# Kernel optimization log

Measured on AMD Instinct MI355X. Metric: run time of the kernel, lower is better.

The kernel has to match this reference:

```python
import jax, jax.numpy as jnp
import numpy as np

B = 16384
INPUT_DIM = 256
NUM_SLOTS = 32
SLOT_DIM = 64
NUM_KNOWN = 9
HIDDEN = 128
ITERS = 3
LN_EPS = 1e-5


def _lin(k, fan_in, w_shape, b_shape):
    # torch nn.Linear default init: U(-1/sqrt(fan_in), 1/sqrt(fan_in))
    bound = 1.0 / np.sqrt(fan_in)
    k1, k2 = jax.random.split(k)
    W = jax.random.uniform(k1, w_shape, jnp.float32, -bound, bound)
    b = jax.random.uniform(k2, b_shape, jnp.float32, -bound, bound)
    return W, b


def setup_inputs() -> dict:
    key = jax.random.key(0)
    ks = jax.random.split(key, 20)
    inp = {}
    inp['world_state'] = jax.random.normal(ks[0], (B, INPUT_DIM), jnp.float32)
    inp['eps'] = jax.random.normal(ks[1], (B, NUM_SLOTS, SLOT_DIM), jnp.float32)
    inp['slots_mu'] = jax.random.normal(ks[2], (1, NUM_SLOTS, SLOT_DIM), jnp.float32)
    inp['slots_sigma'] = jnp.ones((1, NUM_SLOTS, SLOT_DIM), jnp.float32) * 0.1
    inp['Wi'], inp['bi'] = _lin(ks[3], INPUT_DIM, (INPUT_DIM, SLOT_DIM), (SLOT_DIM,))
    inp['Wk'], inp['bk'] = _lin(ks[4], SLOT_DIM, (SLOT_DIM, SLOT_DIM), (SLOT_DIM,))
    inp['Wq'], inp['bq'] = _lin(ks[5], SLOT_DIM, (SLOT_DIM, SLOT_DIM), (SLOT_DIM,))
    inp['Wv'], inp['bv'] = _lin(ks[6], SLOT_DIM, (SLOT_DIM, SLOT_DIM), (SLOT_DIM,))
    inp['W_ih'], inp['b_ih'] = _lin(ks[7], SLOT_DIM, (SLOT_DIM, 3 * SLOT_DIM), (3 * SLOT_DIM,))
    inp['W_hh'], inp['b_hh'] = _lin(ks[8], SLOT_DIM, (SLOT_DIM, 3 * SLOT_DIM), (3 * SLOT_DIM,))
    inp['W1'], inp['b1'] = _lin(ks[9], SLOT_DIM, (SLOT_DIM, HIDDEN), (HIDDEN,))
    inp['W2'], inp['b2'] = _lin(ks[10], HIDDEN, (HIDDEN, SLOT_DIM), (SLOT_DIM,))
    inp['g_in'] = jnp.ones((SLOT_DIM,), jnp.float32)
    inp['b_in'] = jnp.zeros((SLOT_DIM,), jnp.float32)
    inp['g_sl'] = jnp.ones((SLOT_DIM,), jnp.float32)
    inp['b_sl'] = jnp.zeros((SLOT_DIM,), jnp.float32)
    inp['g_mlp'] = jnp.ones((SLOT_DIM,), jnp.float32)
    inp['b_mlp'] = jnp.zeros((SLOT_DIM,), jnp.float32)
    inp['Wh1'], inp['bh1'] = _lin(ks[11], SLOT_DIM, (NUM_KNOWN, SLOT_DIM, SLOT_DIM // 2), (NUM_KNOWN, SLOT_DIM // 2))
    inp['Wh2'], inp['bh2'] = _lin(ks[12], SLOT_DIM // 2, (NUM_KNOWN, SLOT_DIM // 2), (NUM_KNOWN,))
    return inp


def _ln(x, g, b):
    mu = jnp.mean(x, axis=-1, keepdims=True)
    var = jnp.mean(jnp.square(x - mu), axis=-1, keepdims=True)
    return (x - mu) / jnp.sqrt(var + LN_EPS) * g + b


def reference(world_state, eps, slots_mu, slots_sigma, Wi, bi, Wk, bk, Wq, bq, Wv, bv,
              W_ih, b_ih, W_hh, b_hh, W1, b1, W2, b2,
              g_in, b_in, g_sl, b_sl, g_mlp, b_mlp, Wh1, bh1, Wh2, bh2):
    scale = SLOT_DIM ** (-0.5)
    x = world_state[:, None, :] @ Wi + bi            # [B,1,D]
    x = _ln(x, g_in, b_in)
    k = x @ Wk + bk                                   # [B,1,D] (loop-invariant)
    v = x @ Wv + bv                                   # [B,1,D]
    slots = slots_mu + slots_sigma * eps              # [B,S,D]
    for _ in range(ITERS):
        prev = slots
        sn = _ln(slots, g_sl, b_sl)
        q = sn @ Wq + bq                              # [B,S,D]
        attn = jnp.einsum('bnd,bsd->bns', k, q) * scale  # [B,1,S]
        attn = jax.nn.softmax(attn, axis=-1) + 1e-8
        attn = attn / jnp.sum(attn, axis=1, keepdims=True)  # dual normalization
        upd = jnp.einsum('bns,bnd->bsd', attn, v)     # [B,S,D]
        # GRUCell
        gi = upd @ W_ih + b_ih                        # [B,S,3D]
        gh = prev @ W_hh + b_hh
        r = jax.nn.sigmoid(gi[..., :SLOT_DIM] + gh[..., :SLOT_DIM])
        z = jax.nn.sigmoid(gi[..., SLOT_DIM:2 * SLOT_DIM] + gh[..., SLOT_DIM:2 * SLOT_DIM])
        n = jnp.tanh(gi[..., 2 * SLOT_DIM:] + r * gh[..., 2 * SLOT_DIM:])
        slots = (1.0 - z) * n + z * prev
        # residual MLP
        h = _ln(slots, g_mlp, b_mlp)
        slots = slots + jax.nn.gelu(h @ W1 + b1, approximate=False) @ W2 + b2
    # known property heads (vectorized over 9 heads)
    s9 = slots[:, :NUM_KNOWN, :]                      # [B,9,D]
    hh = jax.nn.gelu(jnp.einsum('bkd,kdh->bkh', s9, Wh1) + bh1, approximate=False)
    pv = jax.nn.sigmoid(jnp.einsum('bkh,kh->bk', hh, Wh2) + bh2)  # [B,9]
    free_act = jnp.sqrt(jnp.sum(jnp.square(slots[:, NUM_KNOWN:, :]), axis=-1)).mean(axis=0)  # [num_free]
    return (pv, slots, free_act)
```

## Files before the change

### kernel.cpp

```cpp
#include <hip/hip_runtime.h>


typedef __attribute__((ext_vector_type(4))) float f32x4;
typedef __attribute__((ext_vector_type(8))) short s16x8;

#define MFMA16 __builtin_amdgcn_mfma_f32_16x16x32_bf16

#define NB       16384
#define GIB_OFF  (32 + 120*256)
#define PV_N     147456
#define SLOT_N   33554432

__device__ __forceinline__ unsigned short f2bf(float f){
  unsigned int u = __builtin_bit_cast(unsigned int, f);
  u += 0x7fffu + ((u >> 16) & 1u);
  return (unsigned short)(u >> 16);
}
__device__ __forceinline__ float bf2f(unsigned short s){
  unsigned int u = ((unsigned int)s) << 16;
  return __builtin_bit_cast(float, u);
}
__device__ __forceinline__ float sigm(float x){
  return __builtin_amdgcn_rcpf(1.f + __expf(-x));
}
__device__ __forceinline__ float tanh_(float x){
  return 1.f - 2.f*__builtin_amdgcn_rcpf(1.f + __expf(2.f*x));
}
__device__ __forceinline__ float geluf(float x){
  return x * sigm(1.5957691216f*x*(1.f + 0.044715f*x*x));
}

__global__ void prep1_pack(const float* __restrict__ Wi, const float* __restrict__ Wv,
                           const float* __restrict__ Wih, const float* __restrict__ Whh,
                           const float* __restrict__ W1, const float* __restrict__ W2,
                           float* __restrict__ wsf){
  int t = blockIdx.x*256 + threadIdx.x;
  if (blockIdx.x == 0 && threadIdx.x < 32) wsf[threadIdx.x] = 0.f;
  if (t >= 120*64) return;
  int frag = t >> 6, lane = t & 63;
  int q = lane >> 4, idx = lane & 15;
  const float* W; int ncols, ct, kf;
  if      (frag < 24){ W=Whh; ncols=192; ct=frag>>1;      kf=frag&1; }
  else if (frag < 40){ int f=frag-24; W=W1;  ncols=128; ct=f>>1; kf=f&1; }
  else if (frag < 56){ int f=frag-40; W=W2;  ncols=64;  ct=f>>2; kf=f&3; }
  else if (frag < 88){ int f=frag-56; W=Wi;  ncols=64;  ct=f>>3; kf=f&7; }
  else if (frag < 96){ int f=frag-88; W=Wv;  ncols=64;  ct=f>>1; kf=f&1; }
  else               { int f=frag-96; W=Wih; ncols=192; ct=f>>1; kf=f&1; }
  int k0 = kf*32 + q*8;
  int n  = ct*16 + idx;
  unsigned short* dst = (unsigned short*)(wsf + 32) + frag*512 + lane*8;
  #pragma unroll
  for (int j = 0; j < 8; ++j) dst[j] = f2bf(W[(size_t)(k0+j)*ncols + n]);
}

__global__ __launch_bounds__(256) void prep2_gi(
    const float* __restrict__ wstate, const float* __restrict__ bi,
    const float* __restrict__ bv, const float* __restrict__ bih,
    const float* __restrict__ g_in, const float* __restrict__ b_in,
    float* __restrict__ wsf){
  __shared__ __align__(16) unsigned short sxn[4][1152];
  const f32x4 zf = {0.f,0.f,0.f,0.f};
  int tid = threadIdx.x;
  int w = __builtin_amdgcn_readfirstlane(tid >> 6);
  int lane = tid & 63, q = lane >> 4, idx = lane & 15;
  int br0 = blockIdx.x*64 + w*16;
  const unsigned short* fb = (const unsigned short*)(wsf + 32);
  float* gib = wsf + GIB_OFF;

  s16x8 af[8];
  #pragma unroll
  for (int kf = 0; kf < 8; ++kf){
    const float* src = wstate + (size_t)(br0+idx)*256 + kf*32 + q*8;
    f32x4 p0 = *(const f32x4*)(src);
    f32x4 p1 = *(const f32x4*)(src+4);
    s16x8 a;
    a[0]=(short)f2bf(p0[0]); a[1]=(short)f2bf(p0[1]); a[2]=(short)f2bf(p0[2]); a[3]=(short)f2bf(p0[3]);
    a[4]=(short)f2bf(p1[0]); a[5]=(short)f2bf(p1[1]); a[6]=(short)f2bf(p1[2]); a[7]=(short)f2bf(p1[3]);
    af[kf] = a;
  }
  float xv[4][4];
  #pragma unroll
  for (int ct = 0; ct < 4; ++ct){
    f32x4 acc = zf;
    #pragma unroll
    for (int kf = 0; kf < 8; ++kf)
      acc = MFMA16(af[kf], *(const s16x8*)(fb + (56 + ct*8 + kf)*512 + lane*8), acc, 0,0,0);
    float bb = bi[ct*16+idx];
    #pragma unroll
    for (int e = 0; e < 4; ++e) xv[ct][e] = acc[e] + bb;
  }
  #pragma unroll
  for (int e = 0; e < 4; ++e){
    float s1 = xv[0][e]+xv[1][e]+xv[2][e]+xv[3][e];
    float s2 = xv[0][e]*xv[0][e]+xv[1][e]*xv[1][e]+xv[2][e]*xv[2][e]+xv[3][e]*xv[3][e];
    #pragma unroll
    for (int m = 1; m < 16; m <<= 1){ s1 += __shfl_xor(s1,m); s2 += __shfl_xor(s2,m); }
    float mean = s1*(1.f/64.f);
    float var  = s2*(1.f/64.f) - mean*mean;
    float rs   = __builtin_amdgcn_rsqf(var + 1e-5f);
    #pragma unroll
    for (int ct = 0; ct < 4; ++ct){
      int c = ct*16+idx;
      sxn[w][(q*4+e)*72 + c] = f2bf((xv[ct][e]-mean)*rs*g_in[c] + b_in[c]);
    }
  }
  s16x8 xa0 = *(const s16x8*)(&sxn[w][idx*72 + q*8]);
  s16x8 xa1 = *(const s16x8*)(&sxn[w][idx*72 + 32 + q*8]);
  #pragma unroll
  for (int ct = 0; ct < 4; ++ct){
    f32x4 acc = MFMA16(xa0, *(const s16x8*)(fb + (88 + ct*2 + 0)*512 + lane*8), zf, 0,0,0);
    acc       = MFMA16(xa1, *(const s16x8*)(fb + (88 + ct*2 + 1)*512 + lane*8), acc, 0,0,0);
    float bb = bv[ct*16+idx];
    #pragma unroll
    for (int e = 0; e < 4; ++e) sxn[w][(q*4+e)*72 + ct*16+idx] = f2bf(acc[e] + bb);
  }
  s16x8 va0 = *(const s16x8*)(&sxn[w][idx*72 + q*8]);
  s16x8 va1 = *(const s16x8*)(&sxn[w][idx*72 + 32 + q*8]);
  #pragma unroll
  for (int ct = 0; ct < 12; ++ct){
    f32x4 acc = MFMA16(va0, *(const s16x8*)(fb + (96 + ct*2 + 0)*512 + lane*8), zf, 0,0,0);
    acc       = MFMA16(va1, *(const s16x8*)(fb + (96 + ct*2 + 1)*512 + lane*8), acc, 0,0,0);
    float bb = bih[ct*16+idx];
    #pragma unroll
    for (int e = 0; e < 4; ++e)
      gib[(size_t)(br0 + q*4 + e)*192 + ct*16 + idx] = acc[e] + bb;
  }
}

__global__ __launch_bounds__(256, 2) void bank_main(
    const float* __restrict__ eps, const float* __restrict__ smu, const float* __restrict__ ssig,
    const float* __restrict__ bhh, const float* __restrict__ b1v, const float* __restrict__ b2v,
    const float* __restrict__ g_mlp, const float* __restrict__ b_mlp,
    const float* __restrict__ Wh1, const float* __restrict__ bh1,
    const float* __restrict__ Wh2, const float* __restrict__ bh2,
    float* __restrict__ wsf, float* __restrict__ out){
  __shared__ __align__(16) unsigned short swgt[20480];
  __shared__ __align__(16) unsigned short sbuf[4][2176];
  __shared__ float sgi[2][192];
  __shared__ float sbias[512];
  __shared__ float sfree[2][24];
  const f32x4 zf = {0.f,0.f,0.f,0.f};
  int tid = threadIdx.x;
  int w = __builtin_amdgcn_readfirstlane(tid >> 6);
  int lane = tid & 63, q = lane >> 4, idx = lane & 15;
  int pair = w >> 1, half = w & 1;
  int b = blockIdx.x*2 + pair;
  const unsigned short* fb = (const unsigned short*)(wsf + 32);
  const float* gib = wsf + GIB_OFF;

  {
    const uint4* src = (const uint4*)fb;
    uint4* dst = (uint4*)swgt;
    #pragma unroll
    for (int i = 0; i < 10; ++i) dst[tid + 256*i] = src[tid + 256*i];
  }
  for (int i = tid; i < 512; i += 256){
    float vv;
    if      (i < 192) vv = bhh[i];
    else if (i < 320) vv = b1v[i-192];
    else if (i < 384) vv = b2v[i-320];
    else if (i < 448) vv = g_mlp[i-384];
    else              vv = b_mlp[i-448];
    sbias[i] = vv;
  }
  if (half == 0){
    #pragma unroll
    for (int jj = 0; jj < 3; ++jj) sgi[pair][jj*64+lane] = gib[(size_t)b*192 + jj*64 + lane];
  }
  unsigned short* S = &sbuf[w][0];
  int s0 = half*16;
  #pragma unroll
  for (int rr = 0; rr < 16; ++rr){
    int s = s0 + rr;
    float ev = eps[((size_t)b*32 + s)*64 + lane];
    S[rr*136 + lane] = f2bf(smu[s*64+lane] + ssig[s*64+lane]*ev);
  }
  __syncthreads();

  size_t obase = (size_t)PV_N + ((size_t)b*32 + s0)*64;
  #pragma unroll 1
  for (int it = 0; it < 3; ++it){
    s16x8 a0 = *(const s16x8*)(&S[idx*136 + q*8]);
    s16x8 a1 = *(const s16x8*)(&S[idx*136 + 32 + q*8]);
    f32x4 gacc[12];
    #pragma unroll
    for (int ct = 0; ct < 12; ++ct){
      f32x4 acc = MFMA16(a0, *(const s16x8*)(&swgt[(ct*2+0)*512 + lane*8]), zf, 0,0,0);
      gacc[ct]  = MFMA16(a1, *(const s16x8*)(&swgt[(ct*2+1)*512 + lane*8]), acc, 0,0,0);
    }
    float nsv[4][4];
    #pragma unroll
    for (int ct = 0; ct < 4; ++ct){
      int c = ct*16+idx;
      float bhr = sbias[c], bhz = sbias[64+c], bhn = sbias[128+c];
      float gir = sgi[pair][c], giz = sgi[pair][64+c], gin = sgi[pair][128+c];
      #pragma unroll
      for (int e = 0; e < 4; ++e){
        float r = sigm(gir + gacc[ct][e] + bhr);
        float z = sigm(giz + gacc[4+ct][e] + bhz);
        float n = tanh_(gin + r*(gacc[8+ct][e] + bhn));
        float prev = bf2f(S[(q*4+e)*136 + c]);
        nsv[ct][e] = (1.f - z)*n + z*prev;
      }
    }
    #pragma unroll
    for (int e = 0; e < 4; ++e){
      float s1 = nsv[0][e]+nsv[1][e]+nsv[2][e]+nsv[3][e];
      float s2 = nsv[0][e]*nsv[0][e]+nsv[1][e]*nsv[1][e]+nsv[2][e]*nsv[2][e]+nsv[3][e]*nsv[3][e];
      #pragma unroll
      for (int m = 1; m < 16; m <<= 1){ s1 += __shfl_xor(s1,m); s2 += __shfl_xor(s2,m); }
      float mean = s1*(1.f/64.f);
      float var  = s2*(1.f/64.f) - mean*mean;
      float rs   = __builtin_amdgcn_rsqf(var + 1e-5f);
      #pragma unroll
      for (int ct = 0; ct < 4; ++ct){
        int c = ct*16+idx;
        S[(q*4+e)*136 + c] = f2bf((nsv[ct][e]-mean)*rs*sbias[384+c] + sbias[448+c]);
      }
    }
    s16x8 h0 = *(const s16x8*)(&S[idx*136 + q*8]);
    s16x8 h1 = *(const s16x8*)(&S[idx*136 + 32 + q*8]);
    f32x4 macc[8];
    #pragma unroll
    for (int ct = 0; ct < 8; ++ct){
      f32x4 acc = MFMA16(h0, *(const s16x8*)(&swgt[(24+ct*2+0)*512 + lane*8]), zf, 0,0,0);
      macc[ct]  = MFMA16(h1, *(const s16x8*)(&swgt[(24+ct*2+1)*512 + lane*8]), acc, 0,0,0);
    }
    #pragma unroll
    for (int ct = 0; ct < 8; ++ct){
      int c = ct*16+idx;
      float bb = sbias[192+c];
      #pragma unroll
      for (int e = 0; e < 4; ++e)
        S[(q*4+e)*136 + c] = f2bf(geluf(macc[ct][e] + bb));
    }
    s16x8 t0 = *(const s16x8*)(&S[idx*136 +       q*8]);
    s16x8 t1 = *(const s16x8*)(&S[idx*136 + 32  + q*8]);
    s16x8 t2 = *(const s16x8*)(&S[idx*136 + 64  + q*8]);
    s16x8 t3 = *(const s16x8*)(&S[idx*136 + 96  + q*8]);
    #pragma unroll
    for (int ct = 0; ct < 4; ++ct){
      f32x4 acc = MFMA16(t0, *(const s16x8*)(fb + (40+ct*4+0)*512 + lane*8), zf, 0,0,0);
      acc       = MFMA16(t1, *(const s16x8*)(fb + (40+ct*4+1)*512 + lane*8), acc, 0,0,0);
      acc       = MFMA16(t2, *(const s16x8*)(fb + (40+ct*4+2)*512 + lane*8), acc, 0,0,0);
      acc       = MFMA16(t3, *(const s16x8*)(fb + (40+ct*4+3)*512 + lane*8), acc, 0,0,0);
      int c = ct*16+idx;
      float bb = sbias[320+c];
      #pragma unroll
      for (int e = 0; e < 4; ++e){
        float val = nsv[ct][e] + acc[e] + bb;
        S[(q*4+e)*136 + c] = f2bf(val);
        if (it == 2) out[obase + (size_t)(q*4+e)*64 + c] = val;
      }
    }
  }
  __syncthreads();

  if (half == 0){
    int hh = lane & 31, h2 = lane >> 5;
    #pragma unroll 1
    for (int kb = 0; kb < 5; ++kb){
      int k = kb*2 + h2;
      if (k < 9){
        float a = bh1[k*32 + hh];
        const float* wp = Wh1 + (size_t)k*2048 + hh;
        #pragma unroll 4
        for (int dd = 0; dd < 64; ++dd)
          a += bf2f(S[k*136 + dd]) * wp[dd*32];
        float u = geluf(a);
        float p = u * Wh2[k*32 + hh];
        #pragma unroll
        for (int m = 1; m < 32; m <<= 1) p += __shfl_xor(p, m);
        p = sigm(p + bh2[k]);
        if (hh == 0) out[(size_t)b*9 + k] = p;
      }
    }
  } else {
    const unsigned short* SL = &sbuf[w-1][0];
    #pragma unroll 1
    for (int s = 9; s < 32; ++s){
      const unsigned short* src = (s < 16) ? (SL + s*136) : (S + (s-16)*136);
      float v = bf2f(src[lane]);
      float sq = v*v;
      #pragma unroll
      for (int m = 1; m < 64; m <<= 1) sq += __shfl_xor(sq, m);
      if (lane == 0) sfree[pair][s-9] = sqrtf(sq);
    }
  }
  __syncthreads();
  if (tid < 23) atomicAdd(&wsf[tid], sfree[0][tid] + sfree[1][tid]);
}

__global__ void bank_final(const float* __restrict__ wsf, float* __restrict__ out){
  int t = threadIdx.x;
  if (t < 23) out[(size_t)PV_N + SLOT_N + t] = wsf[t] * (1.f/16384.f);
}

extern "C" void kernel_launch(void* const* d_in, const int* in_sizes, int n_in,
                              void* d_out, int out_size, void* d_ws, size_t ws_size,
                              hipStream_t stream){
  (void)in_sizes; (void)n_in; (void)out_size; (void)ws_size;
  const float* wstate = (const float*)d_in[0];
  const float* eps    = (const float*)d_in[1];
  const float* smu    = (const float*)d_in[2];
  const float* ssig   = (const float*)d_in[3];
  const float* Wi     = (const float*)d_in[4];
  const float* bi     = (const float*)d_in[5];
  const float* Wv     = (const float*)d_in[10];
  const float* bv     = (const float*)d_in[11];
  const float* Wih    = (const float*)d_in[12];
  const float* bih    = (const float*)d_in[13];
  const float* Whh    = (const float*)d_in[14];
  const float* bhh    = (const float*)d_in[15];
  const float* W1     = (const float*)d_in[16];
  const float* b1     = (const float*)d_in[17];
  const float* W2     = (const float*)d_in[18];
  const float* b2     = (const float*)d_in[19];
  const float* g_in   = (const float*)d_in[20];
  const float* b_in   = (const float*)d_in[21];
  const float* g_mlp  = (const float*)d_in[24];
  const float* b_mlp  = (const float*)d_in[25];
  const float* Wh1    = (const float*)d_in[26];
  const float* bh1    = (const float*)d_in[27];
  const float* Wh2    = (const float*)d_in[28];
  const float* bh2    = (const float*)d_in[29];
  float* out = (float*)d_out;
  float* wsf = (float*)d_ws;

  prep1_pack<<<dim3(30),   dim3(256), 0, stream>>>(Wi, Wv, Wih, Whh, W1, W2, wsf);
  prep2_gi  <<<dim3(256),  dim3(256), 0, stream>>>(wstate, bi, bv, bih, g_in, b_in, wsf);
  bank_main <<<dim3(8192), dim3(256), 0, stream>>>(eps, smu, ssig, bhh, b1, b2,
                                                   g_mlp, b_mlp, Wh1, bh1, Wh2, bh2,
                                                   wsf, out);
  bank_final<<<dim3(1),    dim3(64),  0, stream>>>(wsf, out);
}
```

Baseline: 748.6 us.

## Transpose MFMA operands, drop LDS weight staging, split property heads into separate kernel

The main kernel stops copying the weight fragments into shared memory and reads them straight from the packed global buffer. MFMA operands are swapped so each lane owns contiguous columns, which allows vectorized bias loads, packed bf16 stores and a 2-step shuffle reduction for LayerNorm. Removing the large LDS array and raising launch bounds to 4 blocks per CU is meant to increase occupancy. The Wh1 heads move to a new MFMA-based kernel that re-reads the final slots from the output. The free-slot norms are now computed in registers, and the r/z hidden biases are folded into gi during prep. This adds another kernel launch and a global read of the slots, and depends on global and L2 bandwidth for the weight reads.

```diff
diff --git a/kernel.cpp b/kernel.cpp
--- a/kernel.cpp
+++ b/kernel.cpp
@@ -3,11 +3,13 @@
 
 typedef __attribute__((ext_vector_type(4))) float f32x4;
 typedef __attribute__((ext_vector_type(8))) short s16x8;
+typedef __attribute__((ext_vector_type(4))) unsigned u32x4;
 
 #define MFMA16 __builtin_amdgcn_mfma_f32_16x16x32_bf16
 
 #define NB       16384
-#define GIB_OFF  (32 + 120*256)
+#define NFRAG    156
+#define GIB_OFF  (32 + NFRAG*256)
 #define PV_N     147456
 #define SLOT_N   33554432
 
@@ -16,10 +18,13 @@
   u += 0x7fffu + ((u >> 16) & 1u);
   return (unsigned short)(u >> 16);
 }
-__device__ __forceinline__ float bf2f(unsigned short s){
-  unsigned int u = ((unsigned int)s) << 16;
-  return __builtin_bit_cast(float, u);
-}
+__device__ __forceinline__ unsigned pk2(float lo, float hi){
+  unsigned a = __builtin_bit_cast(unsigned, hi) + 0x8000u;
+  unsigned b = __builtin_bit_cast(unsigned, lo) + 0x8000u;
+  return __builtin_amdgcn_perm(a, b, 0x07060302u);
+}
+__device__ __forceinline__ float bflo(unsigned u){ return __builtin_bit_cast(float, u << 16); }
+__device__ __forceinline__ float bfhi(unsigned u){ return __builtin_bit_cast(float, u & 0xffff0000u); }
 __device__ __forceinline__ float sigm(float x){
   return __builtin_amdgcn_rcpf(1.f + __expf(-x));
 }
@@ -33,19 +38,20 @@
 __global__ void prep1_pack(const float* __restrict__ Wi, const float* __restrict__ Wv,
                            const float* __restrict__ Wih, const float* __restrict__ Whh,
                            const float* __restrict__ W1, const float* __restrict__ W2,
-                           float* __restrict__ wsf){
+                           const float* __restrict__ Wh1, float* __restrict__ wsf){
   int t = blockIdx.x*256 + threadIdx.x;
   if (blockIdx.x == 0 && threadIdx.x < 32) wsf[threadIdx.x] = 0.f;
-  if (t >= 120*64) return;
+  if (t >= NFRAG*64) return;
   int frag = t >> 6, lane = t & 63;
   int q = lane >> 4, idx = lane & 15;
   const float* W; int ncols, ct, kf;
-  if      (frag < 24){ W=Whh; ncols=192; ct=frag>>1;      kf=frag&1; }
-  else if (frag < 40){ int f=frag-24; W=W1;  ncols=128; ct=f>>1; kf=f&1; }
-  else if (frag < 56){ int f=frag-40; W=W2;  ncols=64;  ct=f>>2; kf=f&3; }
-  else if (frag < 88){ int f=frag-56; W=Wi;  ncols=64;  ct=f>>3; kf=f&7; }
-  else if (frag < 96){ int f=frag-88; W=Wv;  ncols=64;  ct=f>>1; kf=f&1; }
-  else               { int f=frag-96; W=Wih; ncols=192; ct=f>>1; kf=f&1; }
+  if      (frag < 24){ W=Whh; ncols=192; ct=frag>>1; kf=frag&1; }
+  else if (frag < 40){ int f=frag-24;  W=W1;  ncols=128; ct=f>>1; kf=f&1; }
+  else if (frag < 56){ int f=frag-40;  W=W2;  ncols=64;  ct=f>>2; kf=f&3; }
+  else if (frag < 88){ int f=frag-56;  W=Wi;  ncols=64;  ct=f>>3; kf=f&7; }
+  else if (frag < 96){ int f=frag-88;  W=Wv;  ncols=64;  ct=f>>1; kf=f&1; }
+  else if (frag <120){ int f=frag-96;  W=Wih; ncols=192; ct=f>>1; kf=f&1; }
+  else               { int f=frag-120; W=Wh1 + (size_t)(f>>2)*2048; ncols=32; ct=(f>>1)&1; kf=f&1; }
   int k0 = kf*32 + q*8;
   int n  = ct*16 + idx;
   unsigned short* dst = (unsigned short*)(wsf + 32) + frag*512 + lane*8;
@@ -56,6 +62,7 @@
 __global__ __launch_bounds__(256) void prep2_gi(
     const float* __restrict__ wstate, const float* __restrict__ bi,
     const float* __restrict__ bv, const float* __restrict__ bih,
+    const float* __restrict__ bhh,
     const float* __restrict__ g_in, const float* __restrict__ b_in,
     float* __restrict__ wsf){
   __shared__ __align__(16) unsigned short sxn[4][1152];
@@ -73,10 +80,8 @@
     const float* src = wstate + (size_t)(br0+idx)*256 + kf*32 + q*8;
     f32x4 p0 = *(const f32x4*)(src);
     f32x4 p1 = *(const f32x4*)(src+4);
-    s16x8 a;
-    a[0]=(short)f2bf(p0[0]); a[1]=(short)f2bf(p0[1]); a[2]=(short)f2bf(p0[2]); a[3]=(short)f2bf(p0[3]);
-    a[4]=(short)f2bf(p1[0]); a[5]=(short)f2bf(p1[1]); a[6]=(short)f2bf(p1[2]); a[7]=(short)f2bf(p1[3]);
-    af[kf] = a;
+    u32x4 u = { pk2(p0[0],p0[1]), pk2(p0[2],p0[3]), pk2(p1[0],p1[1]), pk2(p1[2],p1[3]) };
+    af[kf] = __builtin_bit_cast(s16x8, u);
   }
   float xv[4][4];
   #pragma unroll
@@ -120,25 +125,23 @@
   for (int ct = 0; ct < 12; ++ct){
     f32x4 acc = MFMA16(va0, *(const s16x8*)(fb + (96 + ct*2 + 0)*512 + lane*8), zf, 0,0,0);
     acc       = MFMA16(va1, *(const s16x8*)(fb + (96 + ct*2 + 1)*512 + lane*8), acc, 0,0,0);
-    float bb = bih[ct*16+idx];
+    int c = ct*16+idx;
+    float bb = bih[c] + (c < 128 ? bhh[c] : 0.f);
     #pragma unroll
     for (int e = 0; e < 4; ++e)
-      gib[(size_t)(br0 + q*4 + e)*192 + ct*16 + idx] = acc[e] + bb;
-  }
-}
-
-__global__ __launch_bounds__(256, 2) void bank_main(
+      gib[(size_t)(br0 + q*4 + e)*192 + c] = acc[e] + bb;
+  }
+}
+
+__global__ __launch_bounds__(256, 4) void bank_main(
     const float* __restrict__ eps, const float* __restrict__ smu, const float* __restrict__ ssig,
     const float* __restrict__ bhh, const float* __restrict__ b1v, const float* __restrict__ b2v,
     const float* __restrict__ g_mlp, const float* __restrict__ b_mlp,
-    const float* __restrict__ Wh1, const float* __restrict__ bh1,
-    const float* __restrict__ Wh2, const float* __restrict__ bh2,
     float* __restrict__ wsf, float* __restrict__ out){
-  __shared__ __align__(16) unsigned short swgt[20480];
   __shared__ __align__(16) unsigned short sbuf[4][2176];
-  __shared__ float sgi[2][192];
-  __shared__ float sbias[512];
-  __shared__ float sfree[2][24];
+  __shared__ __align__(16) float sgi[2][192];
+  __shared__ __align__(16) float sbias[384];
+  __shared__ float sfree[2][23];
   const f32x4 zf = {0.f,0.f,0.f,0.f};
   int tid = threadIdx.x;
   int w = __builtin_amdgcn_readfirstlane(tid >> 6);
@@ -148,19 +151,13 @@
   const unsigned short* fb = (const unsigned short*)(wsf + 32);
   const float* gib = wsf + GIB_OFF;
 
-  {
-    const uint4* src = (const uint4*)fb;
-    uint4* dst = (uint4*)swgt;
-    #pragma unroll
-    for (int i = 0; i < 10; ++i) dst[tid + 256*i] = src[tid + 256*i];
-  }
-  for (int i = tid; i < 512; i += 256){
+  for (int i = tid; i < 384; i += 256){
     float vv;
-    if      (i < 192) vv = bhh[i];
-    else if (i < 320) vv = b1v[i-192];
-    else if (i < 384) vv = b2v[i-320];
-    else if (i < 448) vv = g_mlp[i-384];
-    else              vv = b_mlp[i-448];
+    if      (i <  64) vv = bhh[128+i];
+    else if (i < 192) vv = b1v[i-64];
+    else if (i < 256) vv = b2v[i-192];
+    else if (i < 320) vv = g_mlp[i-256];
+    else              vv = b_mlp[i-320];
     sbias[i] = vv;
   }
   if (half == 0){
@@ -169,126 +166,165 @@
   }
   unsigned short* S = &sbuf[w][0];
   int s0 = half*16;
-  #pragma unroll
-  for (int rr = 0; rr < 16; ++rr){
-    int s = s0 + rr;
-    float ev = eps[((size_t)b*32 + s)*64 + lane];
-    S[rr*136 + lane] = f2bf(smu[s*64+lane] + ssig[s*64+lane]*ev);
+  {
+    int rbase = (lane >> 5)*8;
+    int col2  = (lane & 31)*2;
+    #pragma unroll
+    for (int rr = 0; rr < 8; ++rr){
+      int r = rbase + rr, s = s0 + r;
+      const float2 ev = *(const float2*)&eps [((size_t)b*32 + s)*64 + col2];
+      const float2 mu = *(const float2*)&smu [s*64 + col2];
+      const float2 sg = *(const float2*)&ssig[s*64 + col2];
+      *(unsigned*)&S[r*136 + col2] = pk2(fmaf(sg.x, ev.x, mu.x), fmaf(sg.y, ev.y, mu.y));
+    }
   }
   __syncthreads();
 
-  size_t obase = (size_t)PV_N + ((size_t)b*32 + s0)*64;
+  size_t slotob = (size_t)PV_N + ((size_t)b*32 + s0)*64;
+  int dq = q*4;
+  float fsq = 0.f;
   #pragma unroll 1
   for (int it = 0; it < 3; ++it){
-    s16x8 a0 = *(const s16x8*)(&S[idx*136 + q*8]);
-    s16x8 a1 = *(const s16x8*)(&S[idx*136 + 32 + q*8]);
+    s16x8 sf0 = *(const s16x8*)(&S[idx*136 +      q*8]);
+    s16x8 sf1 = *(const s16x8*)(&S[idx*136 + 32 + q*8]);
     f32x4 gacc[12];
     #pragma unroll
     for (int ct = 0; ct < 12; ++ct){
-      f32x4 acc = MFMA16(a0, *(const s16x8*)(&swgt[(ct*2+0)*512 + lane*8]), zf, 0,0,0);
-      gacc[ct]  = MFMA16(a1, *(const s16x8*)(&swgt[(ct*2+1)*512 + lane*8]), acc, 0,0,0);
+      f32x4 a   = MFMA16(*(const s16x8*)(fb + (ct*2+0)*512 + lane*8), sf0, zf, 0,0,0);
+      gacc[ct]  = MFMA16(*(const s16x8*)(fb + (ct*2+1)*512 + lane*8), sf1, a,  0,0,0);
     }
     float nsv[4][4];
     #pragma unroll
     for (int ct = 0; ct < 4; ++ct){
-      int c = ct*16+idx;
-      float bhr = sbias[c], bhz = sbias[64+c], bhn = sbias[128+c];
-      float gir = sgi[pair][c], giz = sgi[pair][64+c], gin = sgi[pair][128+c];
+      int d = ct*16 + dq;
+      f32x4 gr = *(const f32x4*)&sgi[pair][d];
+      f32x4 gz = *(const f32x4*)&sgi[pair][64  + d];
+      f32x4 gn = *(const f32x4*)&sgi[pair][128 + d];
+      f32x4 bn = *(const f32x4*)&sbias[d];
+      uint2 pu = *(const uint2*)&S[idx*136 + d];
+      float pvv[4] = { bflo(pu.x), bfhi(pu.x), bflo(pu.y), bfhi(pu.y) };
       #pragma unroll
       for (int e = 0; e < 4; ++e){
-        float r = sigm(gir + gacc[ct][e] + bhr);
-        float z = sigm(giz + gacc[4+ct][e] + bhz);
-        float n = tanh_(gin + r*(gacc[8+ct][e] + bhn));
-        float prev = bf2f(S[(q*4+e)*136 + c]);
-        nsv[ct][e] = (1.f - z)*n + z*prev;
+        float r = sigm(gr[e] + gacc[ct][e]);
+        float z = sigm(gz[e] + gacc[4+ct][e]);
+        float n = tanh_(fmaf(r, gacc[8+ct][e] + bn[e], gn[e]));
+        nsv[ct][e] = fmaf(z, pvv[e] - n, n);
       }
     }
-    #pragma unroll
-    for (int e = 0; e < 4; ++e){
-      float s1 = nsv[0][e]+nsv[1][e]+nsv[2][e]+nsv[3][e];
-      float s2 = nsv[0][e]*nsv[0][e]+nsv[1][e]*nsv[1][e]+nsv[2][e]*nsv[2][e]+nsv[3][e]*nsv[3][e];
+    float s1 = 0.f, s2 = 0.f;
+    #pragma unroll
+    for (int ct = 0; ct < 4; ++ct)
       #pragma unroll
-      for (int m = 1; m < 16; m <<= 1){ s1 += __shfl_xor(s1,m); s2 += __shfl_xor(s2,m); }
-      float mean = s1*(1.f/64.f);
-      float var  = s2*(1.f/64.f) - mean*mean;
-      float rs   = __builtin_amdgcn_rsqf(var + 1e-5f);
+      for (int e = 0; e < 4; ++e){ s1 += nsv[ct][e]; s2 = fmaf(nsv[ct][e], nsv[ct][e], s2); }
+    s1 += __shfl_xor(s1, 16); s2 += __shfl_xor(s2, 16);
+    s1 += __shfl_xor(s1, 32); s2 += __shfl_xor(s2, 32);
+    float mean = s1*(1.f/64.f);
+    float var  = fmaf(-mean, mean, s2*(1.f/64.f));
+    float rs   = __builtin_amdgcn_rsqf(var + 1e-5f);
+    float mrs  = mean*rs;
+    #pragma unroll
+    for (int ct = 0; ct < 4; ++ct){
+      int d = ct*16 + dq;
+      f32x4 gm = *(const f32x4*)&sbias[256 + d];
+      f32x4 bm = *(const f32x4*)&sbias[320 + d];
+      float h[4];
       #pragma unroll
-      for (int ct = 0; ct < 4; ++ct){
-        int c = ct*16+idx;
-        S[(q*4+e)*136 + c] = f2bf((nsv[ct][e]-mean)*rs*sbias[384+c] + sbias[448+c]);
-      }
-    }
-    s16x8 h0 = *(const s16x8*)(&S[idx*136 + q*8]);
+      for (int e = 0; e < 4; ++e)
+        h[e] = fmaf(fmaf(nsv[ct][e], rs, -mrs), gm[e], bm[e]);
+      uint2 uu = { pk2(h[0],h[1]), pk2(h[2],h[3]) };
+      *(uint2*)&S[idx*136 + d] = uu;
+    }
+    s16x8 h0 = *(const s16x8*)(&S[idx*136 +      q*8]);
     s16x8 h1 = *(const s16x8*)(&S[idx*136 + 32 + q*8]);
     f32x4 macc[8];
     #pragma unroll
     for (int ct = 0; ct < 8; ++ct){
-      f32x4 acc = MFMA16(h0, *(const s16x8*)(&swgt[(24+ct*2+0)*512 + lane*8]), zf, 0,0,0);
-      macc[ct]  = MFMA16(h1, *(const s16x8*)(&swgt[(24+ct*2+1)*512 + lane*8]), acc, 0,0,0);
+      f32x4 a  = MFMA16(*(const s16x8*)(fb + (24+ct*2+0)*512 + lane*8), h0, zf, 0,0,0);
+      macc[ct] = MFMA16(*(const s16x8*)(fb + (24+ct*2+1)*512 + lane*8), h1, a,  0,0,0);
     }
     #pragma unroll
     for (int ct = 0; ct < 8; ++ct){
-      int c = ct*16+idx;
-      float bb = sbias[192+c];
+      int d = ct*16 + dq;
+      f32x4 bb = *(const f32x4*)&sbias[64 + d];
+      float tv[4];
       #pragma unroll
-      for (int e = 0; e < 4; ++e)
-        S[(q*4+e)*136 + c] = f2bf(geluf(macc[ct][e] + bb));
-    }
-    s16x8 t0 = *(const s16x8*)(&S[idx*136 +       q*8]);
-    s16x8 t1 = *(const s16x8*)(&S[idx*136 + 32  + q*8]);
-    s16x8 t2 = *(const s16x8*)(&S[idx*136 + 64  + q*8]);
-    s16x8 t3 = *(const s16x8*)(&S[idx*136 + 96  + q*8]);
+      for (int e = 0; e < 4; ++e) tv[e] = geluf(macc[ct][e] + bb[e]);
+      uint2 uu = { pk2(tv[0],tv[1]), pk2(tv[2],tv[3]) };
+      *(uint2*)&S[idx*136 + d] = uu;
+    }
+    s16x8 t0 = *(const s16x8*)(&S[idx*136 +      q*8]);
+    s16x8 t1 = *(const s16x8*)(&S[idx*136 + 32 + q*8]);
+    s16x8 t2 = *(const s16x8*)(&S[idx*136 + 64 + q*8]);
+    s16x8 t3 = *(const s16x8*)(&S[idx*136 + 96 + q*8]);
     #pragma unroll
     for (int ct = 0; ct < 4; ++ct){
-      f32x4 acc = MFMA16(t0, *(const s16x8*)(fb + (40+ct*4+0)*512 + lane*8), zf, 0,0,0);
-      acc       = MFMA16(t1, *(const s16x8*)(fb + (40+ct*4+1)*512 + lane*8), acc, 0,0,0);
-      acc       = MFMA16(t2, *(const s16x8*)(fb + (40+ct*4+2)*512 + lane*8), acc, 0,0,0);
-      acc       = MFMA16(t3, *(const s16x8*)(fb + (40+ct*4+3)*512 + lane*8), acc, 0,0,0);
-      int c = ct*16+idx;
-      float bb = sbias[320+c];
-      #pragma unroll
-      for (int e = 0; e < 4; ++e){
-        float val = nsv[ct][e] + acc[e] + bb;
-        S[(q*4+e)*136 + c] = f2bf(val);
-        if (it == 2) out[obase + (size_t)(q*4+e)*64 + c] = val;
+      f32x4 a = MFMA16(*(const s16x8*)(fb + (40+ct*4+0)*512 + lane*8), t0, zf, 0,0,0);
+      a       = MFMA16(*(const s16x8*)(fb + (40+ct*4+1)*512 + lane*8), t1, a,  0,0,0);
+      a       = MFMA16(*(const s16x8*)(fb + (40+ct*4+2)*512 + lane*8), t2, a,  0,0,0);
+      a       = MFMA16(*(const s16x8*)(fb + (40+ct*4+3)*512 + lane*8), t3, a,  0,0,0);
+      int d = ct*16 + dq;
+      f32x4 bb = *(const f32x4*)&sbias[192 + d];
+      float v0 = nsv[ct][0] + a[0] + bb[0];
+      float v1 = nsv[ct][1] + a[1] + bb[1];
+      float v2 = nsv[ct][2] + a[2] + bb[2];
+      float v3 = nsv[ct][3] + a[3] + bb[3];
+      if (it < 2){
+        uint2 uu = { pk2(v0,v1), pk2(v2,v3) };
+        *(uint2*)&S[idx*136 + d] = uu;
+      } else {
+        f32x4 o = {v0,v1,v2,v3};
+        *(f32x4*)&out[slotob + (size_t)idx*64 + d] = o;
+        fsq = fmaf(v0,v0,fsq); fsq = fmaf(v1,v1,fsq);
+        fsq = fmaf(v2,v2,fsq); fsq = fmaf(v3,v3,fsq);
       }
     }
   }
-  __syncthreads();
-
-  if (half == 0){
-    int hh = lane & 31, h2 = lane >> 5;
-    #pragma unroll 1
-    for (int kb = 0; kb < 5; ++kb){
-      int k = kb*2 + h2;
-      if (k < 9){
-        float a = bh1[k*32 + hh];
-        const float* wp = Wh1 + (size_t)k*2048 + hh;
-        #pragma unroll 4
-        for (int dd = 0; dd < 64; ++dd)
-          a += bf2f(S[k*136 + dd]) * wp[dd*32];
-        float u = geluf(a);
-        float p = u * Wh2[k*32 + hh];
-        #pragma unroll
-        for (int m = 1; m < 32; m <<= 1) p += __shfl_xor(p, m);
-        p = sigm(p + bh2[k]);
-        if (hh == 0) out[(size_t)b*9 + k] = p;
-      }
-    }
-  } else {
-    const unsigned short* SL = &sbuf[w-1][0];
-    #pragma unroll 1
-    for (int s = 9; s < 32; ++s){
-      const unsigned short* src = (s < 16) ? (SL + s*136) : (S + (s-16)*136);
-      float v = bf2f(src[lane]);
-      float sq = v*v;
-      #pragma unroll
-      for (int m = 1; m < 64; m <<= 1) sq += __shfl_xor(sq, m);
-      if (lane == 0) sfree[pair][s-9] = sqrtf(sq);
-    }
-  }
+  fsq += __shfl_xor(fsq, 16);
+  fsq += __shfl_xor(fsq, 32);
+  int srow = s0 + idx;
+  if (q == 0 && srow >= 9) sfree[pair][srow-9] = sqrtf(fsq);
   __syncthreads();
   if (tid < 23) atomicAdd(&wsf[tid], sfree[0][tid] + sfree[1][tid]);
+}
+
+__global__ __launch_bounds__(256) void pv_head(
+    const float* __restrict__ bh1, const float* __restrict__ Wh2,
+    const float* __restrict__ bh2, const float* __restrict__ wsf,
+    float* __restrict__ out){
+  const f32x4 zf = {0.f,0.f,0.f,0.f};
+  int tid = threadIdx.x, w = tid >> 6, lane = tid & 63;
+  int q = lane >> 4, idx = lane & 15;
+  int wid = blockIdx.x*4 + w;
+  int k = wid % 9, b0 = (wid/9)*16;
+  const unsigned short* fb = (const unsigned short*)(wsf + 32);
+  const float* slots = out + PV_N;
+  s16x8 af[2];
+  #pragma unroll
+  for (int kf = 0; kf < 2; ++kf){
+    const float* sp = slots + ((size_t)(b0+idx)*32 + k)*64 + kf*32 + q*8;
+    f32x4 p0 = *(const f32x4*)sp;
+    f32x4 p1 = *(const f32x4*)(sp+4);
+    u32x4 u = { pk2(p0[0],p0[1]), pk2(p0[2],p0[3]), pk2(p1[0],p1[1]), pk2(p1[2],p1[3]) };
+    af[kf] = __builtin_bit_cast(s16x8, u);
+  }
+  float g[2][4];
+  #pragma unroll
+  for (int ct = 0; ct < 2; ++ct){
+    f32x4 a = MFMA16(af[0], *(const s16x8*)(fb + (120+k*4+ct*2+0)*512 + lane*8), zf, 0,0,0);
+    a       = MFMA16(af[1], *(const s16x8*)(fb + (120+k*4+ct*2+1)*512 + lane*8), a,  0,0,0);
+    float bb = bh1[k*32 + ct*16 + idx];
+    #pragma unroll
+    for (int e = 0; e < 4; ++e) g[ct][e] = geluf(a[e] + bb);
+  }
+  float w0 = Wh2[k*32 + idx], w1 = Wh2[k*32 + 16 + idx];
+  float bk = bh2[k];
+  #pragma unroll
+  for (int e = 0; e < 4; ++e){
+    float p = fmaf(g[1][e], w1, g[0][e]*w0);
+    #pragma unroll
+    for (int m = 1; m < 16; m <<= 1) p += __shfl_xor(p, m);
+    if (idx == 0) out[(size_t)(b0 + q*4 + e)*9 + k] = sigm(p + bk);
+  }
 }
 
 __global__ void bank_final(const float* __restrict__ wsf, float* __restrict__ out){
@@ -327,10 +363,10 @@
   float* out = (float*)d_out;
   float* wsf = (float*)d_ws;
 
-  prep1_pack<<<dim3(30),   dim3(256), 0, stream>>>(Wi, Wv, Wih, Whh, W1, W2, wsf);
-  prep2_gi  <<<dim3(256),  dim3(256), 0, stream>>>(wstate, bi, bv, bih, g_in, b_in, wsf);
+  prep1_pack<<<dim3(39),   dim3(256), 0, stream>>>(Wi, Wv, Wih, Whh, W1, W2, Wh1, wsf);
+  prep2_gi  <<<dim3(256),  dim3(256), 0, stream>>>(wstate, bi, bv, bih, bhh, g_in, b_in, wsf);
   bank_main <<<dim3(8192), dim3(256), 0, stream>>>(eps, smu, ssig, bhh, b1, b2,
-                                                   g_mlp, b_mlp, Wh1, bh1, Wh2, bh2,
-                                                   wsf, out);
+                                                   g_mlp, b_mlp, wsf, out);
+  pv_head   <<<dim3(2304), dim3(256), 0, stream>>>(bh1, Wh2, bh2, wsf, out);
   bank_final<<<dim3(1),    dim3(64),  0, stream>>>(wsf, out);
 }
```

New measurement: 2.394 ms. 220% more time.
